# Kernel tuning notes

Measured on AMD Instinct MI355X. Metric: run time of the kernel, lower is better.

The kernel has to match this reference:

```python
import jax, jax.numpy as jnp
import numpy as np

N_NODES = 50000
N_EDGES = 800000
IN_F = 128
OUT_F = 64


def setup_inputs() -> dict:
    key = jax.random.key(0)
    k1, k2, k3, k4, k5 = jax.random.split(key, 5)
    x = jax.random.normal(k1, (N_NODES, IN_F), dtype=jnp.float32)
    edge_index = jax.random.randint(k2, (2, N_EDGES), 0, N_NODES, dtype=jnp.int64)
    edge_weight = jax.random.uniform(k3, (N_EDGES,), dtype=jnp.float32)
    # Linear(in,out,bias=False): store as [in, out] so h = x @ W
    W = jax.random.normal(k4, (IN_F, OUT_F), dtype=jnp.float32) * (1.0 / np.sqrt(IN_F))
    # Linear(2*out, 1, bias=False): store as [2*out] vector
    a = jax.random.normal(k5, (2 * OUT_F,), dtype=jnp.float32) * (1.0 / np.sqrt(2 * OUT_F))
    return {"x": x, "edge_index": edge_index, "edge_weight": edge_weight, "W": W, "a": a}


def reference(x, edge_index, edge_weight, W, a):
    N = x.shape[0]
    F = W.shape[1]
    src, dst = edge_index[0], edge_index[1]
    h = x @ W  # [N, F]
    # a([h_src ; h_dst]) == h_src @ a[:F] + h_dst @ a[F:]  (no edge-level concat)
    s_src = h @ a[:F]   # [N]
    s_dst = h @ a[F:]   # [N]
    e = s_src[src] + s_dst[dst]            # [E]
    alpha = jax.nn.leaky_relu(e, negative_slope=0.2) * edge_weight
    alpha = alpha - jnp.max(alpha)         # global max subtraction, as in source
    alpha_exp = jnp.exp(alpha)             # [E]
    alpha_sum = jax.ops.segment_sum(alpha_exp, dst, num_segments=N)  # [N]
    alpha_norm = alpha_exp / (alpha_sum[dst] + 1e-8)                 # [E] (dropout = identity, eval mode)
    out = jax.ops.segment_sum(h[src] * alpha_norm[:, None], dst, num_segments=N)  # [N, F]
    return jax.nn.elu(out)
```

## Files before the change

### kernel.cpp

```cpp
#include <hip/hip_runtime.h>
#include <hip/hip_bf16.h>
#include <math.h>

#define FIN 128
#define FOUT 64
#define TM 64
#define XPAD 4

#define DB 64
#define CAP 1280
#define NBMAX 1024
#define TILE_A 2048
#define EPT_A 8

static __device__ __forceinline__ unsigned short f2bf(float f) {
  __hip_bfloat16 b = __float2bfloat16(f);
  return *reinterpret_cast<unsigned short*>(&b);
}

__global__ __launch_bounds__(256) void k_gemm(
    const float* __restrict__ x, const float* __restrict__ W,
    const float* __restrict__ a, unsigned short* __restrict__ hbf,
    float* __restrict__ s_src, float* __restrict__ s_dst, int N)
{
  __shared__ float xs[TM][FIN + XPAD];
  __shared__ float Ws[FIN][FOUT];
  int t = threadIdx.x;
  int n0 = blockIdx.x * TM;

#pragma unroll
  for (int i = 0; i < 8; i++) {
    int idx = t + i * 256;
    int row = idx >> 5, c4 = (idx & 31) * 4;
    int n = n0 + row;
    float4 v = make_float4(0.f, 0.f, 0.f, 0.f);
    if (n < N) v = *(const float4*)&x[(size_t)n * FIN + c4];
    *(float4*)&xs[row][c4] = v;
  }
#pragma unroll
  for (int i = 0; i < 8; i++) {
    int idx = t + i * 256;
    int row = idx >> 4, c4 = (idx & 15) * 4;
    *(float4*)&Ws[row][c4] = *(const float4*)&W[row * FOUT + c4];
  }
  __syncthreads();

  int tx = t & 15, ty = t >> 4;
  float acc[4][4];
#pragma unroll
  for (int r = 0; r < 4; r++)
#pragma unroll
    for (int c = 0; c < 4; c++) acc[r][c] = 0.f;

  for (int k0 = 0; k0 < FIN; k0 += 4) {
    float4 wr[4], xr[4];
#pragma unroll
    for (int i = 0; i < 4; i++) wr[i] = *(float4*)&Ws[k0 + i][tx * 4];
#pragma unroll
    for (int r = 0; r < 4; r++) xr[r] = *(float4*)&xs[ty * 4 + r][k0];
#pragma unroll
    for (int r = 0; r < 4; r++) {
      float xv[4] = {xr[r].x, xr[r].y, xr[r].z, xr[r].w};
#pragma unroll
      for (int i = 0; i < 4; i++) {
        acc[r][0] = fmaf(xv[i], wr[i].x, acc[r][0]);
        acc[r][1] = fmaf(xv[i], wr[i].y, acc[r][1]);
        acc[r][2] = fmaf(xv[i], wr[i].z, acc[r][2]);
        acc[r][3] = fmaf(xv[i], wr[i].w, acc[r][3]);
      }
    }
  }

  int f0 = tx * 4;
  float a1[4], a2[4];
#pragma unroll
  for (int c = 0; c < 4; c++) { a1[c] = a[f0 + c]; a2[c] = a[FOUT + f0 + c]; }

#pragma unroll
  for (int r = 0; r < 4; r++) {
    int n = n0 + ty * 4 + r;
    float c1 = acc[r][0] * a1[0] + acc[r][1] * a1[1] +
               acc[r][2] * a1[2] + acc[r][3] * a1[3];
    float c2 = acc[r][0] * a2[0] + acc[r][1] * a2[1] +
               acc[r][2] * a2[2] + acc[r][3] * a2[3];
#pragma unroll
    for (int o = 1; o < 16; o <<= 1) {
      c1 += __shfl_xor(c1, o);
      c2 += __shfl_xor(c2, o);
    }
    if (n < N) {
      ushort4 u = make_ushort4(f2bf(acc[r][0]), f2bf(acc[r][1]),
                               f2bf(acc[r][2]), f2bf(acc[r][3]));
      *(ushort4*)&hbf[(size_t)n * FOUT + f0] = u;
      if (tx == 0) { s_src[n] = c1; s_dst[n] = c2; }
    }
  }
}

__global__ __launch_bounds__(256) void k_bucketA(
    const int* __restrict__ src, const int* __restrict__ dst,
    const float* __restrict__ ew, const float* __restrict__ s_src,
    const float* __restrict__ s_dst, int* __restrict__ bcur,
    uint2* __restrict__ inter, int E, int nbuck)
{
  __shared__ uint2 stage[TILE_A];
  __shared__ int hist[NBMAX];
  __shared__ int sbase[NBMAX];
  __shared__ int gbase[NBMAX];
  __shared__ int wsum[4];

  int t = threadIdx.x;
  int base = blockIdx.x * TILE_A;
  int cntTile = E - base; if (cntTile > TILE_A) cntTile = TILE_A;

  for (int i = t; i < nbuck; i += 256) hist[i] = 0;
  __syncthreads();

  unsigned key[EPT_A]; float aev[EPT_A]; int lpos[EPT_A];
#pragma unroll
  for (int i = 0; i < EPT_A; i++) {
    int e = base + t + i * 256;
    lpos[i] = -1;
    if (e < E) {
      int s = src[e], d = dst[e];
      float v = s_src[s] + s_dst[d];
      v = (v > 0.f) ? v : 0.2f * v;
      v *= ew[e];
      key[i] = ((unsigned)d << 16) | (unsigned)s;
      aev[i] = expf(v);
      lpos[i] = atomicAdd(&hist[d >> 6], 1);
    }
  }
  __syncthreads();

  int i0 = t * 4;
  int c0 = (i0 + 0 < nbuck) ? hist[i0 + 0] : 0;
  int c1 = (i0 + 1 < nbuck) ? hist[i0 + 1] : 0;
  int c2 = (i0 + 2 < nbuck) ? hist[i0 + 2] : 0;
  int c3 = (i0 + 3 < nbuck) ? hist[i0 + 3] : 0;
  int ts = c0 + c1 + c2 + c3;
  int lane = t & 63, wid = t >> 6;
  int inc = ts;
#pragma unroll
  for (int o = 1; o < 64; o <<= 1) {
    int up = __shfl_up(inc, o);
    if (lane >= o) inc += up;
  }
  if (lane == 63) wsum[wid] = inc;
  __syncthreads();
  int woff = 0;
  for (int w = 0; w < wid; w++) woff += wsum[w];
  int run = woff + inc - ts;
  if (i0 + 0 < nbuck) sbase[i0 + 0] = run; run += c0;
  if (i0 + 1 < nbuck) sbase[i0 + 1] = run; run += c1;
  if (i0 + 2 < nbuck) sbase[i0 + 2] = run; run += c2;
  if (i0 + 3 < nbuck) sbase[i0 + 3] = run;
  __syncthreads();

  for (int b = t; b < nbuck; b += 256)
    if (hist[b] > 0) gbase[b] = atomicAdd(&bcur[b], hist[b]);
  __syncthreads();

#pragma unroll
  for (int i = 0; i < EPT_A; i++)
    if (lpos[i] >= 0) {
      int b = key[i] >> 22;
      stage[sbase[b] + lpos[i]] = make_uint2(key[i], __float_as_uint(aev[i]));
    }
  __syncthreads();

  for (int i = t; i < cntTile; i += 256) {
    uint2 en = stage[i];
    int b = en.x >> 22;
    int slot = gbase[b] + (i - sbase[b]);
    if (slot < CAP) inter[(size_t)b * CAP + slot] = en;
  }
}

__global__ __launch_bounds__(512) void k_bucketB(
    const uint2* __restrict__ inter, const int* __restrict__ bcur,
    const unsigned short* __restrict__ hbf, float* __restrict__ out, int N)
{
  __shared__ uint2 ss[CAP];
  __shared__ int hist[DB];
  __shared__ int rp[DB];
  int b = blockIdx.x;
  int t = threadIdx.x;
  int cnt = bcur[b]; if (cnt > CAP) cnt = CAP;

  if (t < DB) hist[t] = 0;
  __syncthreads();

  const uint2* bin = inter + (size_t)b * CAP;
  unsigned kx[3], ka[3]; int lp[3], dl[3];
#pragma unroll
  for (int i = 0; i < 3; i++) {
    int p = t + i * 512;
    lp[i] = -1;
    if (p < cnt) {
      uint2 en = bin[p];
      kx[i] = en.x; ka[i] = en.y;
      dl[i] = (en.x >> 16) & (DB - 1);
      lp[i] = atomicAdd(&hist[dl[i]], 1);
    }
  }
  __syncthreads();

  if (t < DB) {
    int v = hist[t];
    int inc = v;
#pragma unroll
    for (int o = 1; o < 64; o <<= 1) {
      int up = __shfl_up(inc, o);
      if (t >= o) inc += up;
    }
    rp[t] = inc - v;
  }
  __syncthreads();

#pragma unroll
  for (int i = 0; i < 3; i++)
    if (lp[i] >= 0) ss[rp[dl[i]] + lp[i]] = make_uint2(kx[i], ka[i]);
  __syncthreads();

  int grp = t >> 3, l = t & 7;
  int n = b * DB + grp;
  int beg = rp[grp];
  int end = beg + hist[grp];

  float acc[8];
#pragma unroll
  for (int i = 0; i < 8; i++) acc[i] = 0.f;
  float asum = 0.f;

  for (int p = beg; p < end; p += 2) {
    uint2 e0 = ss[p];
    float ae0 = __uint_as_float(e0.y);
    uint4 r0 = ((const uint4*)(hbf + ((size_t)(e0.x & 0xFFFFu) << 6)))[l];
    float ae1 = 0.f;
    uint4 r1 = make_uint4(0u, 0u, 0u, 0u);
    if (p + 1 < end) {
      uint2 e1 = ss[p + 1];
      ae1 = __uint_as_float(e1.y);
      r1 = ((const uint4*)(hbf + ((size_t)(e1.x & 0xFFFFu) << 6)))[l];
    }
    asum += ae0 + ae1;
    const unsigned* u0 = (const unsigned*)&r0;
    const unsigned* u1 = (const unsigned*)&r1;
#pragma unroll
    for (int i = 0; i < 4; i++) {
      float2 f0 = __bfloat1622float2(*(const __hip_bfloat162*)&u0[i]);
      float2 f1 = __bfloat1622float2(*(const __hip_bfloat162*)&u1[i]);
      acc[2 * i]     = fmaf(ae0, f0.x, acc[2 * i]);
      acc[2 * i + 1] = fmaf(ae0, f0.y, acc[2 * i + 1]);
      acc[2 * i]     = fmaf(ae1, f1.x, acc[2 * i]);
      acc[2 * i + 1] = fmaf(ae1, f1.y, acc[2 * i + 1]);
    }
  }

  if (n < N) {
    float inv = 1.f / (asum + 1e-8f);
    float v[8];
#pragma unroll
    for (int i = 0; i < 8; i++) {
      v[i] = acc[i] * inv;
      v[i] = (v[i] > 0.f) ? v[i] : expm1f(v[i]);
    }
    float* op = &out[(size_t)n * FOUT + l * 8];
    *(float4*)op       = make_float4(v[0], v[1], v[2], v[3]);
    *(float4*)(op + 4) = make_float4(v[4], v[5], v[6], v[7]);
  }
}

extern "C" void kernel_launch(void* const* d_in, const int* in_sizes, int n_in,
                              void* d_out, int out_size, void* d_ws, size_t ws_size,
                              hipStream_t stream)
{
  const float* x  = (const float*)d_in[0];
  const int*   ei = (const int*)d_in[1];
  const float* ew = (const float*)d_in[2];
  const float* W  = (const float*)d_in[3];
  const float* a  = (const float*)d_in[4];
  float* out = (float*)d_out;

  const int N = in_sizes[0] / FIN;
  const int E = in_sizes[2];
  const int* src = ei;
  const int* dst = ei + E;
  const int nbuck = (N + DB - 1) / DB;

  unsigned short* hbf = (unsigned short*)d_ws;
  float* ssrc  = (float*)(hbf + (size_t)N * FOUT);
  float* sdst  = ssrc + N;
  int*   bcur  = (int*)(sdst + N);
  uint2* inter = (uint2*)(bcur + 800);

  hipMemsetAsync(bcur, 0, (size_t)nbuck * sizeof(int), stream);

  k_gemm<<<(N + TM - 1) / TM, 256, 0, stream>>>(x, W, a, hbf, ssrc, sdst, N);
  k_bucketA<<<(E + TILE_A - 1) / TILE_A, 256, 0, stream>>>(src, dst, ew, ssrc, sdst, bcur, inter, E, nbuck);
  k_bucketB<<<nbuck, 512, 0, stream>>>(inter, bcur, hbf, out, N);
}
```

Baseline: 140.7 us.

## Use bf16 MFMA for feature GEMM and fold attention vector into W

```diff
diff --git a/kernel.cpp b/kernel.cpp
--- a/kernel.cpp
+++ b/kernel.cpp
@@ -5,7 +5,7 @@
 #define FIN 128
 #define FOUT 64
 #define TM 64
-#define XPAD 4
+#define XS_STRIDE 136
 
 #define DB 64
 #define CAP 1280
@@ -13,20 +13,49 @@
 #define TILE_A 2048
 #define EPT_A 8
 
+typedef __attribute__((ext_vector_type(8))) short short8;
+typedef __attribute__((ext_vector_type(4))) float floatx4;
+
 static __device__ __forceinline__ unsigned short f2bf(float f) {
   __hip_bfloat16 b = __float2bfloat16(f);
   return *reinterpret_cast<unsigned short*>(&b);
 }
 
+__global__ __launch_bounds__(256) void k_prep(
+    const float* __restrict__ W, const float* __restrict__ a,
+    unsigned short* __restrict__ Wt, float* __restrict__ Wa,
+    int* __restrict__ bcur, int nbuck)
+{
+  int t = threadIdx.x, b = blockIdx.x;
+  int gid = b * 256 + t;
+  int stride = gridDim.x * 256;
+  for (int i = gid; i < nbuck; i += stride) bcur[i] = 0;
+  for (int i = gid; i < FIN * FOUT; i += stride) {
+    int f = i >> 7, k = i & 127;
+    Wt[i] = f2bf(W[k * FOUT + f]);
+  }
+  if (b == 0) {
+    int which = t >> 7, k = t & 127;
+    const float* av = a + which * FOUT;
+    const float* wr = W + k * FOUT;
+    float c = 0.f;
+#pragma unroll
+    for (int f = 0; f < FOUT; f++) c = fmaf(wr[f], av[f], c);
+    Wa[which * FIN + k] = c;
+  }
+}
+
 __global__ __launch_bounds__(256) void k_gemm(
-    const float* __restrict__ x, const float* __restrict__ W,
-    const float* __restrict__ a, unsigned short* __restrict__ hbf,
+    const float* __restrict__ x, const unsigned short* __restrict__ Wt,
+    const float* __restrict__ Wa, unsigned short* __restrict__ hbf,
     float* __restrict__ s_src, float* __restrict__ s_dst, int N)
 {
-  __shared__ float xs[TM][FIN + XPAD];
-  __shared__ float Ws[FIN][FOUT];
+  __shared__ unsigned short xsb[TM][XS_STRIDE];
+  __shared__ float wa[2][FIN];
   int t = threadIdx.x;
   int n0 = blockIdx.x * TM;
+
+  wa[t >> 7][t & 127] = Wa[t];
 
 #pragma unroll
   for (int i = 0; i < 8; i++) {
@@ -35,66 +64,62 @@
     int n = n0 + row;
     float4 v = make_float4(0.f, 0.f, 0.f, 0.f);
     if (n < N) v = *(const float4*)&x[(size_t)n * FIN + c4];
-    *(float4*)&xs[row][c4] = v;
-  }
-#pragma unroll
-  for (int i = 0; i < 8; i++) {
-    int idx = t + i * 256;
-    int row = idx >> 4, c4 = (idx & 15) * 4;
-    *(float4*)&Ws[row][c4] = *(const float4*)&W[row * FOUT + c4];
-  }
-  __syncthreads();
-
-  int tx = t & 15, ty = t >> 4;
-  float acc[4][4];
-#pragma unroll
-  for (int r = 0; r < 4; r++)
-#pragma unroll
-    for (int c = 0; c < 4; c++) acc[r][c] = 0.f;
-
-  for (int k0 = 0; k0 < FIN; k0 += 4) {
-    float4 wr[4], xr[4];
-#pragma unroll
-    for (int i = 0; i < 4; i++) wr[i] = *(float4*)&Ws[k0 + i][tx * 4];
-#pragma unroll
-    for (int r = 0; r < 4; r++) xr[r] = *(float4*)&xs[ty * 4 + r][k0];
+    ushort4 u = make_ushort4(f2bf(v.x), f2bf(v.y), f2bf(v.z), f2bf(v.w));
+    *(ushort4*)&xsb[row][c4] = u;
+  }
+  __syncthreads();
+
+  {
+    int row = t >> 2, which = (t >> 1) & 1, half = t & 1;
+    int n = n0 + row;
+    float c = 0.f;
+    if (n < N) {
+      const float4* xr = (const float4*)&x[(size_t)n * FIN + half * 64];
+      const float* wv = &wa[which][half * 64];
+#pragma unroll
+      for (int kk = 0; kk < 16; kk++) {
+        float4 xv = xr[kk];
+        c = fmaf(xv.x, wv[kk * 4 + 0],
+            fmaf(xv.y, wv[kk * 4 + 1],
+            fmaf(xv.z, wv[kk * 4 + 2],
+            fmaf(xv.w, wv[kk * 4 + 3], c))));
+      }
+    }
+    c += __shfl_xor(c, 1);
+    if (half == 0 && n < N) {
+      if (which == 0) s_src[n] = c; else s_dst[n] = c;
+    }
+  }
+
+  int lane = t & 63, w = t >> 6;
+  int m = lane & 15, q = lane >> 4;
+
+  short8 bf[4][4];
+#pragma unroll
+  for (int k0 = 0; k0 < 4; k0++)
+#pragma unroll
+    for (int j = 0; j < 4; j++)
+      bf[k0][j] = *(const short8*)(Wt + (j * 16 + m) * FIN + k0 * 32 + q * 8);
+
+  floatx4 acc[4];
+#pragma unroll
+  for (int j = 0; j < 4; j++) acc[j] = (floatx4){0.f, 0.f, 0.f, 0.f};
+
+#pragma unroll
+  for (int k0 = 0; k0 < 4; k0++) {
+    short8 af = *(const short8*)&xsb[w * 16 + m][k0 * 32 + q * 8];
+#pragma unroll
+    for (int j = 0; j < 4; j++)
+      acc[j] = __builtin_amdgcn_mfma_f32_16x16x32_bf16(af, bf[k0][j], acc[j], 0, 0, 0);
+  }
+
+#pragma unroll
+  for (int j = 0; j < 4; j++)
 #pragma unroll
     for (int r = 0; r < 4; r++) {
-      float xv[4] = {xr[r].x, xr[r].y, xr[r].z, xr[r].w};
-#pragma unroll
-      for (int i = 0; i < 4; i++) {
-        acc[r][0] = fmaf(xv[i], wr[i].x, acc[r][0]);
-        acc[r][1] = fmaf(xv[i], wr[i].y, acc[r][1]);
-        acc[r][2] = fmaf(xv[i], wr[i].z, acc[r][2]);
-        acc[r][3] = fmaf(xv[i], wr[i].w, acc[r][3]);
-      }
-    }
-  }
-
-  int f0 = tx * 4;
-  float a1[4], a2[4];
-#pragma unroll
-  for (int c = 0; c < 4; c++) { a1[c] = a[f0 + c]; a2[c] = a[FOUT + f0 + c]; }
-
-#pragma unroll
-  for (int r = 0; r < 4; r++) {
-    int n = n0 + ty * 4 + r;
-    float c1 = acc[r][0] * a1[0] + acc[r][1] * a1[1] +
-               acc[r][2] * a1[2] + acc[r][3] * a1[3];
-    float c2 = acc[r][0] * a2[0] + acc[r][1] * a2[1] +
-               acc[r][2] * a2[2] + acc[r][3] * a2[3];
-#pragma unroll
-    for (int o = 1; o < 16; o <<= 1) {
-      c1 += __shfl_xor(c1, o);
-      c2 += __shfl_xor(c2, o);
-    }
-    if (n < N) {
-      ushort4 u = make_ushort4(f2bf(acc[r][0]), f2bf(acc[r][1]),
-                               f2bf(acc[r][2]), f2bf(acc[r][3]));
-      *(ushort4*)&hbf[(size_t)n * FOUT + f0] = u;
-      if (tx == 0) { s_src[n] = c1; s_dst[n] = c2; }
-    }
-  }
+      int n = n0 + w * 16 + q * 4 + r;
+      if (n < N) hbf[(size_t)n * FOUT + j * 16 + m] = f2bf(acc[j][r]);
+    }
 }
 
 __global__ __launch_bounds__(256) void k_bucketA(
@@ -289,15 +314,16 @@
   const int* dst = ei + E;
   const int nbuck = (N + DB - 1) / DB;
 
-  unsigned short* hbf = (unsigned short*)d_ws;
+  unsigned short* Wt = (unsigned short*)d_ws;
+  float* Wa    = (float*)(Wt + FIN * FOUT);
+  unsigned short* hbf = (unsigned short*)(Wa + 256);
   float* ssrc  = (float*)(hbf + (size_t)N * FOUT);
   float* sdst  = ssrc + N;
   int*   bcur  = (int*)(sdst + N);
   uint2* inter = (uint2*)(bcur + 800);
 
-  hipMemsetAsync(bcur, 0, (size_t)nbuck * sizeof(int), stream);
-
-  k_gemm<<<(N + TM - 1) / TM, 256, 0, stream>>>(x, W, a, hbf, ssrc, sdst, N);
+  k_prep<<<33, 256, 0, stream>>>(W, a, Wt, Wa, bcur, nbuck);
+  k_gemm<<<(N + TM - 1) / TM, 256, 0, stream>>>(x, Wt, Wa, hbf, ssrc, sdst, N);
   k_bucketA<<<(E + TILE_A - 1) / TILE_A, 256, 0, stream>>>(src, dst, ew, ssrc, sdst, bcur, inter, E, nbuck);
   k_bucketB<<<nbuck, 512, 0, stream>>>(inter, bcur, hbf, out, N);
 }
```

Result: faster. 136.4 us (-3.1%).
